# Kernel tuning notes

Measured on AMD Instinct MI355X. Metric: run time of the kernel, lower is better.

The kernel has to match this reference:

```python
import jax, jax.numpy as jnp
import numpy as np

IN_DIM, OUT_DIM = 256, 128
N_NODES, N_EDGES = 50000, 800000


def _glorot(key, shape):
    fan_in = shape[-1]
    return jax.random.normal(key, shape, dtype=jnp.float32) / jnp.sqrt(jnp.float32(fan_in))


def setup_inputs() -> dict:
    key = jax.random.key(0)
    ks = jax.random.split(key, 16)
    features1 = jax.random.normal(ks[0], (N_NODES, IN_DIM), dtype=jnp.float32)
    edge_index = jax.random.randint(ks[1], (2, N_EDGES), 0, N_NODES, dtype=jnp.int32)
    return {
        "features1": features1,
        "edge_index": edge_index,
        # encoder conv1: in->out
        "Wl_e1": _glorot(ks[2], (OUT_DIM, IN_DIM)), "bl_e1": jnp.zeros((OUT_DIM,), jnp.float32), "Wr_e1": _glorot(ks[3], (OUT_DIM, IN_DIM)),
        # encoder conv2: out->out
        "Wl_e2": _glorot(ks[4], (OUT_DIM, OUT_DIM)), "bl_e2": jnp.zeros((OUT_DIM,), jnp.float32), "Wr_e2": _glorot(ks[5], (OUT_DIM, OUT_DIM)),
        # fc: out->out
        "W_fc": _glorot(ks[6], (OUT_DIM, OUT_DIM)), "b_fc": jnp.zeros((OUT_DIM,), jnp.float32),
        # decoder conv1: out->out
        "Wl_d1": _glorot(ks[7], (OUT_DIM, OUT_DIM)), "bl_d1": jnp.zeros((OUT_DIM,), jnp.float32), "Wr_d1": _glorot(ks[8], (OUT_DIM, OUT_DIM)),
        # decoder conv2: out->in
        "Wl_d2": _glorot(ks[9], (IN_DIM, OUT_DIM)), "bl_d2": jnp.zeros((IN_DIM,), jnp.float32), "Wr_d2": _glorot(ks[10], (IN_DIM, OUT_DIM)),
    }


def _sage_conv(x, src, dst, inv_deg, Wl, bl, Wr):
    # mean aggregation of neighbor messages x[src] at destination nodes
    agg = jax.ops.segment_sum(x[src], dst, num_segments=N_NODES) * inv_deg  # [N, d_in]
    out = agg @ Wl.T + bl + x @ Wr.T  # lin_l(agg) + lin_r(x)
    # F.normalize(out, p=2, dim=-1)
    nrm = jnp.maximum(jnp.linalg.norm(out, axis=-1, keepdims=True), 1e-12)
    return out / nrm


def reference(features1, edge_index, Wl_e1, bl_e1, Wr_e1, Wl_e2, bl_e2, Wr_e2,
              W_fc, b_fc, Wl_d1, bl_d1, Wr_d1, Wl_d2, bl_d2, Wr_d2):
    src, dst = edge_index[0], edge_index[1]
    deg = jax.ops.segment_sum(jnp.ones((src.shape[0],), jnp.float32), dst, num_segments=N_NODES)
    inv_deg = (1.0 / jnp.maximum(deg, 1.0))[:, None]
    # encoder
    h = _sage_conv(features1, src, dst, inv_deg, Wl_e1, bl_e1, Wr_e1)
    x1 = _sage_conv(h, src, dst, inv_deg, Wl_e2, bl_e2, Wr_e2)
    # bottleneck linear
    x = x1 @ W_fc.T + b_fc
    # decoder
    h = _sage_conv(x, src, dst, inv_deg, Wl_d1, bl_d1, Wr_d1)
    x1_rec = _sage_conv(h, src, dst, inv_deg, Wl_d2, bl_d2, Wr_d2)
    return (x1, x1_rec)
```

## Files before the change

### kernel.cpp

```cpp
#include <hip/hip_runtime.h>
#include <hip/hip_bf16.h>
#include <math.h>

#define N_NODES 50000
#define N_EDGES 800000
#define SLOT_CAP 64

typedef short s16x8 __attribute__((ext_vector_type(8)));
typedef float f32x4 __attribute__((ext_vector_type(4)));

static __device__ __forceinline__ unsigned short f2bf(float x) {
    __hip_bfloat16 b = __float2bfloat16(x);
    return *(unsigned short*)&b;
}
static __device__ __forceinline__ float2 bfu2f2(unsigned int u) {
    __hip_bfloat162 b = *(__hip_bfloat162*)&u;
    return __bfloat1622float2(b);
}
static __device__ __forceinline__ unsigned int packbf2(float x, float y) {
    return (unsigned int)f2bf(x) | ((unsigned int)f2bf(y) << 16);
}

__global__ void k_fillslot(const int* __restrict__ src, const int* __restrict__ dst,
                           int* __restrict__ cnt, int* __restrict__ slots) {
    int e = blockIdx.x * blockDim.x + threadIdx.x;
    if (e >= N_EDGES) return;
    int d = dst[e];
    int pos = atomicAdd(&cnt[d], 1);
    if (pos < SLOT_CAP) slots[d * SLOT_CAP + pos] = src[e];
}

#define FEATN (N_NODES * 256)
#define O_WL_E1 (FEATN)
#define O_WR_E1 (FEATN + 32768)
#define O_WL_E2 (FEATN + 65536)
#define O_WR_E2 (FEATN + 81920)
#define O_W_FC  (FEATN + 98304)
#define O_WL_D1 (FEATN + 114688)
#define O_WR_D1 (FEATN + 131072)
#define O_D2    (FEATN + 147456)
#define PREP_TOT (FEATN + 212992)

__global__ __launch_bounds__(256) void k_prep(const float* __restrict__ feat,
                                              const float* __restrict__ wle1, const float* __restrict__ wre1,
                                              const float* __restrict__ wle2, const float* __restrict__ wre2,
                                              const float* __restrict__ wfc,
                                              const float* __restrict__ wld1, const float* __restrict__ wrd1,
                                              const float* __restrict__ wld2, const float* __restrict__ wrd2,
                                              unsigned short* __restrict__ dstp) {
    const int tot4 = PREP_TOT / 4;
    for (int i = blockIdx.x * blockDim.x + threadIdx.x; i < tot4; i += gridDim.x * blockDim.x) {
        int e = i * 4;
        const float* s;
        int off;
        if      (e < O_WL_E1) { s = feat; off = e; }
        else if (e < O_WR_E1) { s = wle1; off = e - O_WL_E1; }
        else if (e < O_WL_E2) { s = wre1; off = e - O_WR_E1; }
        else if (e < O_WR_E2) { s = wle2; off = e - O_WL_E2; }
        else if (e < O_W_FC)  { s = wre2; off = e - O_WR_E2; }
        else if (e < O_WL_D1) { s = wfc;  off = e - O_W_FC; }
        else if (e < O_WR_D1) { s = wld1; off = e - O_WL_D1; }
        else if (e < O_D2)    { s = wrd1; off = e - O_WR_D1; }
        else {
            int rel = e - O_D2;
            int row = rel >> 8, half = (rel >> 7) & 1, col = rel & 127;
            s = half ? wrd2 : wld2;
            off = row * 128 + col;
        }
        float4 v = *(const float4*)&s[off];
        ushort4 u;
        u.x = f2bf(v.x); u.y = f2bf(v.y); u.z = f2bf(v.z); u.w = f2bf(v.w);
        *(ushort4*)&dstp[e] = u;
    }
}

template <int K>
__global__ __launch_bounds__(256) void k_gmm2(const unsigned short* __restrict__ X,
                                              const unsigned short* __restrict__ W,
                                              const float* __restrict__ bias0,
                                              const float* __restrict__ bias1,
                                              unsigned short* __restrict__ Y,
                                              int N, int Ystride) {
    constexpr int CH = K / 8;
    __shared__ unsigned short Ws[128 * K];
    const unsigned short* Wsrc = W + (size_t)blockIdx.y * 128 * K;
    for (int idx = threadIdx.x; idx < 128 * CH; idx += 256) {
        int n = idx / CH, c = idx % CH;
        uint4 v = *(const uint4*)&Wsrc[n * K + c * 8];
        int cs = c ^ (n & 15);
        *(uint4*)&Ws[n * K + cs * 8] = v;
    }
    __syncthreads();

    const int wid = threadIdx.x >> 6, lane = threadIdx.x & 63;
    const int row0 = blockIdx.x * 128 + wid * 32;
    const int lrow = lane & 15;
    const int lk8  = lane >> 4;
    f32x4 acc[2][8] = {};

    for (int ks = 0; ks < K; ks += 32) {
        s16x8 a[2];
#pragma unroll
        for (int i = 0; i < 2; i++) {
            int r = row0 + i * 16 + lrow;
            s16x8 av = {};
            if (r < N) av = *(const s16x8*)&X[(size_t)r * K + ks + lk8 * 8];
            a[i] = av;
        }
#pragma unroll
        for (int nf = 0; nf < 8; nf++) {
            int n = nf * 16 + lrow;
            int c = (ks >> 3) + lk8;
            int cs = c ^ (n & 15);
            s16x8 b = *(const s16x8*)&Ws[n * K + cs * 8];
            acc[0][nf] = __builtin_amdgcn_mfma_f32_16x16x32_bf16(a[0], b, acc[0][nf], 0, 0, 0);
            acc[1][nf] = __builtin_amdgcn_mfma_f32_16x16x32_bf16(a[1], b, acc[1][nf], 0, 0, 0);
        }
    }

    const float* bias = (blockIdx.y == 0) ? bias0 : bias1;
    const int ccol = lane & 15, crow0 = (lane >> 4) * 4;
    const int ycol0 = blockIdx.y * 128;
#pragma unroll
    for (int nf = 0; nf < 8; nf++) {
        int lcol = nf * 16 + ccol;
        float bv = bias ? bias[lcol] : 0.0f;
#pragma unroll
        for (int i = 0; i < 2; i++) {
#pragma unroll
            for (int j = 0; j < 4; j++) {
                int grow = row0 + i * 16 + crow0 + j;
                if (grow < N) Y[(size_t)grow * Ystride + ycol0 + lcol] = f2bf(acc[i][nf][j] + bv);
            }
        }
    }
}

template <bool WRITE_F32>
__global__ __launch_bounds__(256) void k_aggfin4(const uint4* __restrict__ TP,
                                                 const int* __restrict__ slots,
                                                 const int* __restrict__ cnt,
                                                 float* __restrict__ OUTF,
                                                 uint4* __restrict__ OUTB,
                                                 int ostride4, int ooff4) {
    const int wave = (blockIdx.x * blockDim.x + threadIdx.x) >> 6;
    const int lane = threadIdx.x & 63;
    if (wave >= N_NODES) return;
    const int q = lane & 15, sub = lane >> 4;
    int deg = cnt[wave];
    deg = min(deg, SLOT_CAP);
    const int base = wave * SLOT_CAP;
    float acc[8] = {};
    int i = sub;
    for (; i + 4 < deg; i += 8) {
        int nb0 = slots[base + i], nb1 = slots[base + i + 4];
        uint4 v0 = TP[(size_t)nb0 * 32 + q];
        uint4 v1 = TP[(size_t)nb1 * 32 + q];
        float2 a0 = bfu2f2(v0.x), a1 = bfu2f2(v0.y), a2 = bfu2f2(v0.z), a3 = bfu2f2(v0.w);
        float2 b0 = bfu2f2(v1.x), b1 = bfu2f2(v1.y), b2 = bfu2f2(v1.z), b3 = bfu2f2(v1.w);
        acc[0] += a0.x + b0.x; acc[1] += a0.y + b0.y;
        acc[2] += a1.x + b1.x; acc[3] += a1.y + b1.y;
        acc[4] += a2.x + b2.x; acc[5] += a2.y + b2.y;
        acc[6] += a3.x + b3.x; acc[7] += a3.y + b3.y;
    }
    if (i < deg) {
        int nb = slots[base + i];
        uint4 v = TP[(size_t)nb * 32 + q];
        float2 a0 = bfu2f2(v.x), a1 = bfu2f2(v.y), a2 = bfu2f2(v.z), a3 = bfu2f2(v.w);
        acc[0] += a0.x; acc[1] += a0.y; acc[2] += a1.x; acc[3] += a1.y;
        acc[4] += a2.x; acc[5] += a2.y; acc[6] += a3.x; acc[7] += a3.y;
    }
#pragma unroll
    for (int k = 0; k < 8; k++) {
        acc[k] += __shfl_xor(acc[k], 16);
        acc[k] += __shfl_xor(acc[k], 32);
    }
    const float inv = 1.0f / fmaxf((float)deg, 1.0f);
    uint4 pv = TP[(size_t)wave * 32 + 16 + q];
    float2 p0 = bfu2f2(pv.x), p1 = bfu2f2(pv.y), p2 = bfu2f2(pv.z), p3 = bfu2f2(pv.w);
    float o[8];
    o[0] = p0.x + inv * acc[0]; o[1] = p0.y + inv * acc[1];
    o[2] = p1.x + inv * acc[2]; o[3] = p1.y + inv * acc[3];
    o[4] = p2.x + inv * acc[4]; o[5] = p2.y + inv * acc[5];
    o[6] = p3.x + inv * acc[6]; o[7] = p3.y + inv * acc[7];
    float ss = 0.0f;
#pragma unroll
    for (int k = 0; k < 8; k++) ss += o[k] * o[k];
    ss += __shfl_xor(ss, 1); ss += __shfl_xor(ss, 2);
    ss += __shfl_xor(ss, 4); ss += __shfl_xor(ss, 8);
    float r = 1.0f / fmaxf(sqrtf(ss), 1e-12f);
#pragma unroll
    for (int k = 0; k < 8; k++) o[k] *= r;
    if (lane < 16) {
        if constexpr (WRITE_F32) {
            ((float4*)OUTF)[(size_t)wave * 32 + q * 2]     = make_float4(o[0], o[1], o[2], o[3]);
            ((float4*)OUTF)[(size_t)wave * 32 + q * 2 + 1] = make_float4(o[4], o[5], o[6], o[7]);
        }
        uint4 u;
        u.x = packbf2(o[0], o[1]); u.y = packbf2(o[2], o[3]);
        u.z = packbf2(o[4], o[5]); u.w = packbf2(o[6], o[7]);
        OUTB[(size_t)wave * ostride4 + ooff4 + q] = u;
    }
}

__global__ __launch_bounds__(256) void k_agg4(const uint4* __restrict__ IN,
                                              const int* __restrict__ slots,
                                              const int* __restrict__ cnt,
                                              uint4* __restrict__ OUT,
                                              int istride4, int ioff4, int ostride4, int ooff4) {
    const int wave = (blockIdx.x * blockDim.x + threadIdx.x) >> 6;
    const int lane = threadIdx.x & 63;
    if (wave >= N_NODES) return;
    const int q = lane & 15, sub = lane >> 4;
    int deg = cnt[wave];
    deg = min(deg, SLOT_CAP);
    const int base = wave * SLOT_CAP;
    float acc[8] = {};
    int i = sub;
    for (; i + 4 < deg; i += 8) {
        int nb0 = slots[base + i], nb1 = slots[base + i + 4];
        uint4 v0 = IN[(size_t)nb0 * istride4 + ioff4 + q];
        uint4 v1 = IN[(size_t)nb1 * istride4 + ioff4 + q];
        float2 a0 = bfu2f2(v0.x), a1 = bfu2f2(v0.y), a2 = bfu2f2(v0.z), a3 = bfu2f2(v0.w);
        float2 b0 = bfu2f2(v1.x), b1 = bfu2f2(v1.y), b2 = bfu2f2(v1.z), b3 = bfu2f2(v1.w);
        acc[0] += a0.x + b0.x; acc[1] += a0.y + b0.y;
        acc[2] += a1.x + b1.x; acc[3] += a1.y + b1.y;
        acc[4] += a2.x + b2.x; acc[5] += a2.y + b2.y;
        acc[6] += a3.x + b3.x; acc[7] += a3.y + b3.y;
    }
    if (i < deg) {
        int nb = slots[base + i];
        uint4 v = IN[(size_t)nb * istride4 + ioff4 + q];
        float2 a0 = bfu2f2(v.x), a1 = bfu2f2(v.y), a2 = bfu2f2(v.z), a3 = bfu2f2(v.w);
        acc[0] += a0.x; acc[1] += a0.y; acc[2] += a1.x; acc[3] += a1.y;
        acc[4] += a2.x; acc[5] += a2.y; acc[6] += a3.x; acc[7] += a3.y;
    }
#pragma unroll
    for (int k = 0; k < 8; k++) {
        acc[k] += __shfl_xor(acc[k], 16);
        acc[k] += __shfl_xor(acc[k], 32);
    }
    const float inv = 1.0f / fmaxf((float)deg, 1.0f);
    if (lane < 16) {
        uint4 u;
        u.x = packbf2(inv * acc[0], inv * acc[1]);
        u.y = packbf2(inv * acc[2], inv * acc[3]);
        u.z = packbf2(inv * acc[4], inv * acc[5]);
        u.w = packbf2(inv * acc[6], inv * acc[7]);
        OUT[(size_t)wave * ostride4 + ooff4 + q] = u;
    }
}

__global__ __launch_bounds__(256) void k_norm256(const unsigned short* __restrict__ Rb,
                                                 float* __restrict__ OUT) {
    const int wave = (blockIdx.x * blockDim.x + threadIdx.x) >> 6;
    const int lane = threadIdx.x & 63;
    if (wave >= N_NODES) return;
    ushort4 v = ((const ushort4*)Rb)[(size_t)wave * 64 + lane];
    float x0 = __bfloat162float(*(__hip_bfloat16*)&v.x);
    float x1 = __bfloat162float(*(__hip_bfloat16*)&v.y);
    float x2 = __bfloat162float(*(__hip_bfloat16*)&v.z);
    float x3 = __bfloat162float(*(__hip_bfloat16*)&v.w);
    float ss = x0 * x0 + x1 * x1 + x2 * x2 + x3 * x3;
#pragma unroll
    for (int off = 32; off > 0; off >>= 1) ss += __shfl_xor(ss, off);
    float r = 1.0f / fmaxf(sqrtf(ss), 1e-12f);
    float4 o = make_float4(x0 * r, x1 * r, x2 * r, x3 * r);
    ((float4*)OUT)[(size_t)wave * 64 + lane] = o;
}

extern "C" void kernel_launch(void* const* d_in, const int* in_sizes, int n_in,
                              void* d_out, int out_size, void* d_ws, size_t ws_size,
                              hipStream_t stream) {
    const float* feat  = (const float*)d_in[0];
    const int*   ei    = (const int*)d_in[1];
    const int*   src   = ei;
    const int*   dst   = ei + N_EDGES;
    const float* Wl_e1 = (const float*)d_in[2];
    const float* bl_e1 = (const float*)d_in[3];
    const float* Wr_e1 = (const float*)d_in[4];
    const float* Wl_e2 = (const float*)d_in[5];
    const float* bl_e2 = (const float*)d_in[6];
    const float* Wr_e2 = (const float*)d_in[7];
    const float* W_fc  = (const float*)d_in[8];
    const float* b_fc  = (const float*)d_in[9];
    const float* Wl_d1 = (const float*)d_in[10];
    const float* bl_d1 = (const float*)d_in[11];
    const float* Wr_d1 = (const float*)d_in[12];
    const float* Wl_d2 = (const float*)d_in[13];
    const float* bl_d2 = (const float*)d_in[14];
    const float* Wr_d2 = (const float*)d_in[15];

    char* w = (char*)d_ws;
    auto alloc = [&](size_t bytes) -> void* {
        void* p = (void*)w;
        w += (bytes + 255) & ~(size_t)255;
        return p;
    };
    int* cnt   = (int*)alloc((size_t)N_NODES * 4);
    int* slots = (int*)alloc((size_t)N_NODES * SLOT_CAP * 4);
    unsigned short* bfpool = (unsigned short*)alloc((size_t)PREP_TOT * 2);
    unsigned short* TP   = (unsigned short*)alloc((size_t)N_NODES * 256 * 2);
    unsigned short* hb   = (unsigned short*)alloc((size_t)N_NODES * 128 * 2);
    unsigned short* x1b  = (unsigned short*)alloc((size_t)N_NODES * 128 * 2);
    unsigned short* X2   = (unsigned short*)alloc((size_t)N_NODES * 256 * 2);
    unsigned short* R1b  = (unsigned short*)alloc((size_t)N_NODES * 256 * 2);

    unsigned short* featb = bfpool;
    float* x1     = (float*)d_out;
    float* x1_rec = (float*)d_out + (size_t)N_NODES * 128;

    hipMemsetAsync(cnt, 0, (size_t)N_NODES * 4, stream);

    const int EB = (N_EDGES + 255) / 256;
    k_prep<<<2048, 256, 0, stream>>>(feat, Wl_e1, Wr_e1, Wl_e2, Wr_e2, W_fc, Wl_d1, Wr_d1, Wl_d2, Wr_d2, bfpool);
    k_fillslot<<<EB, 256, 0, stream>>>(src, dst, cnt, slots);

    const int NB128 = (N_NODES + 127) / 128;
    const int WPB   = (N_NODES * 64 + 255) / 256;

    k_gmm2<256><<<dim3(NB128, 2), 256, 0, stream>>>(featb, bfpool + O_WL_E1, nullptr, bl_e1, TP, N_NODES, 256);
    k_aggfin4<false><<<WPB, 256, 0, stream>>>((const uint4*)TP, slots, cnt, nullptr, (uint4*)hb, 16, 0);
    k_gmm2<128><<<dim3(NB128, 2), 256, 0, stream>>>(hb, bfpool + O_WL_E2, nullptr, bl_e2, TP, N_NODES, 256);
    k_aggfin4<true><<<WPB, 256, 0, stream>>>((const uint4*)TP, slots, cnt, x1, (uint4*)x1b, 16, 0);
    k_gmm2<128><<<dim3(NB128, 1), 256, 0, stream>>>(x1b, bfpool + O_W_FC, b_fc, nullptr, hb, N_NODES, 128);
    k_gmm2<128><<<dim3(NB128, 2), 256, 0, stream>>>(hb, bfpool + O_WL_D1, nullptr, bl_d1, TP, N_NODES, 256);
    k_aggfin4<false><<<WPB, 256, 0, stream>>>((const uint4*)TP, slots, cnt, nullptr, (uint4*)X2, 32, 16);
    k_agg4<<<WPB, 256, 0, stream>>>((const uint4*)X2, slots, cnt, (uint4*)X2, 32, 16, 32, 0);
    k_gmm2<256><<<dim3(NB128, 2), 256, 0, stream>>>(X2, bfpool + O_D2, bl_d2, bl_d2 + 128, R1b, N_NODES, 256);
    k_norm256<<<WPB, 256, 0, stream>>>(R1b, x1_rec);
}
```

Baseline: 341.3 us.

## Build compact CSR via bucketed counting sort and prefetch A tiles in GEMM

Replaces the fixed 64-slot per-node adjacency (filled with per-node global atomics) with a compact CSR. Edges are first bucketed into 256-node bins, then an exclusive scan produces bin offsets and a per-bin LDS counting sort writes row_start and csr. This cuts global atomic contention and makes neighbor index reads contiguous, at the cost of two extra kernel launches and extra passes over the edges. The GEMM kernel also double-buffers the A-operand register loads so the next k-slice is fetched while MFMAs run on the current one.

```diff
diff --git a/kernel.cpp b/kernel.cpp
--- a/kernel.cpp
+++ b/kernel.cpp
@@ -4,7 +4,8 @@
 
 #define N_NODES 50000
 #define N_EDGES 800000
-#define SLOT_CAP 64
+#define NBUCK ((N_NODES + 255) / 256)
+#define BCAP 6144
 
 typedef short s16x8 __attribute__((ext_vector_type(8)));
 typedef float f32x4 __attribute__((ext_vector_type(4)));
@@ -21,13 +22,70 @@
     return (unsigned int)f2bf(x) | ((unsigned int)f2bf(y) << 16);
 }
 
-__global__ void k_fillslot(const int* __restrict__ src, const int* __restrict__ dst,
-                           int* __restrict__ cnt, int* __restrict__ slots) {
+__global__ void k_bucket(const int* __restrict__ src, const int* __restrict__ dst,
+                         int* __restrict__ bcnt, unsigned int* __restrict__ bke) {
     int e = blockIdx.x * blockDim.x + threadIdx.x;
     if (e >= N_EDGES) return;
     int d = dst[e];
-    int pos = atomicAdd(&cnt[d], 1);
-    if (pos < SLOT_CAP) slots[d * SLOT_CAP + pos] = src[e];
+    int b = d >> 8;
+    int pos = atomicAdd(&bcnt[b], 1);
+    if (pos < BCAP) bke[b * BCAP + pos] = (unsigned int)src[e] | ((unsigned int)(d & 255) << 16);
+}
+
+__global__ __launch_bounds__(256) void k_bscan(const int* __restrict__ bcnt, int* __restrict__ bbase) {
+    __shared__ int lds[256];
+    int t = threadIdx.x;
+    int v = (t < NBUCK) ? min(bcnt[t], BCAP) : 0;
+    lds[t] = v;
+    __syncthreads();
+    for (int off = 1; off < 256; off <<= 1) {
+        int x = (t >= off) ? lds[t - off] : 0;
+        __syncthreads();
+        lds[t] += x;
+        __syncthreads();
+    }
+    if (t < NBUCK) bbase[t] = lds[t] - v;
+}
+
+__global__ __launch_bounds__(256) void k_binsort(const unsigned int* __restrict__ bke,
+                                                 const int* __restrict__ bcnt,
+                                                 const int* __restrict__ bbase,
+                                                 int* __restrict__ csr,
+                                                 int* __restrict__ row_start) {
+    __shared__ int cnt_l[256];
+    __shared__ int scan_l[256];
+    __shared__ int cursor[256];
+    __shared__ int stage[BCAP];
+    const int b = blockIdx.x;
+    const int t = threadIdx.x;
+    const int nb = min(bcnt[b], BCAP);
+    const unsigned int* ed = bke + (size_t)b * BCAP;
+    cnt_l[t] = 0;
+    __syncthreads();
+    for (int i = t; i < nb; i += 256) atomicAdd(&cnt_l[(ed[i] >> 16) & 255], 1);
+    __syncthreads();
+    int v = cnt_l[t];
+    scan_l[t] = v;
+    __syncthreads();
+    for (int off = 1; off < 256; off <<= 1) {
+        int x = (t >= off) ? scan_l[t - off] : 0;
+        __syncthreads();
+        scan_l[t] += x;
+        __syncthreads();
+    }
+    int excl = scan_l[t] - v;
+    cursor[t] = excl;
+    const int base = bbase[b];
+    int node = b * 256 + t;
+    if (node <= N_NODES) row_start[node] = base + excl;
+    __syncthreads();
+    for (int i = t; i < nb; i += 256) {
+        unsigned int u = ed[i];
+        int pos = atomicAdd(&cursor[(u >> 16) & 255], 1);
+        stage[pos] = (int)(u & 0xFFFF);
+    }
+    __syncthreads();
+    for (int i = t; i < nb; i += 256) csr[base + i] = stage[i];
 }
 
 #define FEATN (N_NODES * 256)
@@ -98,14 +156,24 @@
     const int lk8  = lane >> 4;
     f32x4 acc[2][8] = {};
 
+    s16x8 a_cur[2];
+#pragma unroll
+    for (int i = 0; i < 2; i++) {
+        int r = row0 + i * 16 + lrow;
+        s16x8 av = {};
+        if (r < N) av = *(const s16x8*)&X[(size_t)r * K + lk8 * 8];
+        a_cur[i] = av;
+    }
+
+#pragma unroll
     for (int ks = 0; ks < K; ks += 32) {
-        s16x8 a[2];
-#pragma unroll
-        for (int i = 0; i < 2; i++) {
-            int r = row0 + i * 16 + lrow;
-            s16x8 av = {};
-            if (r < N) av = *(const s16x8*)&X[(size_t)r * K + ks + lk8 * 8];
-            a[i] = av;
+        s16x8 a_nxt[2] = {};
+        if (ks + 32 < K) {
+#pragma unroll
+            for (int i = 0; i < 2; i++) {
+                int r = row0 + i * 16 + lrow;
+                if (r < N) a_nxt[i] = *(const s16x8*)&X[(size_t)r * K + ks + 32 + lk8 * 8];
+            }
         }
 #pragma unroll
         for (int nf = 0; nf < 8; nf++) {
@@ -113,9 +181,11 @@
             int c = (ks >> 3) + lk8;
             int cs = c ^ (n & 15);
             s16x8 b = *(const s16x8*)&Ws[n * K + cs * 8];
-            acc[0][nf] = __builtin_amdgcn_mfma_f32_16x16x32_bf16(a[0], b, acc[0][nf], 0, 0, 0);
-            acc[1][nf] = __builtin_amdgcn_mfma_f32_16x16x32_bf16(a[1], b, acc[1][nf], 0, 0, 0);
+            acc[0][nf] = __builtin_amdgcn_mfma_f32_16x16x32_bf16(a_cur[0], b, acc[0][nf], 0, 0, 0);
+            acc[1][nf] = __builtin_amdgcn_mfma_f32_16x16x32_bf16(a_cur[1], b, acc[1][nf], 0, 0, 0);
         }
+        a_cur[0] = a_nxt[0];
+        a_cur[1] = a_nxt[1];
     }
 
     const float* bias = (blockIdx.y == 0) ? bias0 : bias1;
@@ -138,8 +208,8 @@
 
 template <bool WRITE_F32>
 __global__ __launch_bounds__(256) void k_aggfin4(const uint4* __restrict__ TP,
-                                                 const int* __restrict__ slots,
-                                                 const int* __restrict__ cnt,
+                                                 const int* __restrict__ csr,
+                                                 const int* __restrict__ row_start,
                                                  float* __restrict__ OUTF,
                                                  uint4* __restrict__ OUTB,
                                                  int ostride4, int ooff4) {
@@ -147,13 +217,12 @@
     const int lane = threadIdx.x & 63;
     if (wave >= N_NODES) return;
     const int q = lane & 15, sub = lane >> 4;
-    int deg = cnt[wave];
-    deg = min(deg, SLOT_CAP);
-    const int base = wave * SLOT_CAP;
+    const int base = row_start[wave];
+    const int deg = row_start[wave + 1] - base;
     float acc[8] = {};
     int i = sub;
     for (; i + 4 < deg; i += 8) {
-        int nb0 = slots[base + i], nb1 = slots[base + i + 4];
+        int nb0 = csr[base + i], nb1 = csr[base + i + 4];
         uint4 v0 = TP[(size_t)nb0 * 32 + q];
         uint4 v1 = TP[(size_t)nb1 * 32 + q];
         float2 a0 = bfu2f2(v0.x), a1 = bfu2f2(v0.y), a2 = bfu2f2(v0.z), a3 = bfu2f2(v0.w);
@@ -164,7 +233,7 @@
         acc[6] += a3.x + b3.x; acc[7] += a3.y + b3.y;
     }
     if (i < deg) {
-        int nb = slots[base + i];
+        int nb = csr[base + i];
         uint4 v = TP[(size_t)nb * 32 + q];
         float2 a0 = bfu2f2(v.x), a1 = bfu2f2(v.y), a2 = bfu2f2(v.z), a3 = bfu2f2(v.w);
         acc[0] += a0.x; acc[1] += a0.y; acc[2] += a1.x; acc[3] += a1.y;
@@ -204,21 +273,20 @@
 }
 
 __global__ __launch_bounds__(256) void k_agg4(const uint4* __restrict__ IN,
-                                              const int* __restrict__ slots,
-                                              const int* __restrict__ cnt,
+                                              const int* __restrict__ csr,
+                                              const int* __restrict__ row_start,
                                               uint4* __restrict__ OUT,
                                               int istride4, int ioff4, int ostride4, int ooff4) {
     const int wave = (blockIdx.x * blockDim.x + threadIdx.x) >> 6;
     const int lane = threadIdx.x & 63;
     if (wave >= N_NODES) return;
     const int q = lane & 15, sub = lane >> 4;
-    int deg = cnt[wave];
-    deg = min(deg, SLOT_CAP);
-    const int base = wave * SLOT_CAP;
+    const int base = row_start[wave];
+    const int deg = row_start[wave + 1] - base;
     float acc[8] = {};
     int i = sub;
     for (; i + 4 < deg; i += 8) {
-        int nb0 = slots[base + i], nb1 = slots[base + i + 4];
+        int nb0 = csr[base + i], nb1 = csr[base + i + 4];
         uint4 v0 = IN[(size_t)nb0 * istride4 + ioff4 + q];
         uint4 v1 = IN[(size_t)nb1 * istride4 + ioff4 + q];
         float2 a0 = bfu2f2(v0.x), a1 = bfu2f2(v0.y), a2 = bfu2f2(v0.z), a3 = bfu2f2(v0.w);
@@ -229,7 +297,7 @@
         acc[6] += a3.x + b3.x; acc[7] += a3.y + b3.y;
     }
     if (i < deg) {
-        int nb = slots[base + i];
+        int nb = csr[base + i];
         uint4 v = IN[(size_t)nb * istride4 + ioff4 + q];
         float2 a0 = bfu2f2(v.x), a1 = bfu2f2(v.y), a2 = bfu2f2(v.z), a3 = bfu2f2(v.w);
         acc[0] += a0.x; acc[1] += a0.y; acc[2] += a1.x; acc[3] += a1.y;
@@ -297,8 +365,11 @@
         w += (bytes + 255) & ~(size_t)255;
         return p;
     };
-    int* cnt   = (int*)alloc((size_t)N_NODES * 4);
-    int* slots = (int*)alloc((size_t)N_NODES * SLOT_CAP * 4);
+    int* bcnt      = (int*)alloc((size_t)NBUCK * 4);
+    int* bbase     = (int*)alloc((size_t)NBUCK * 4);
+    unsigned int* bke = (unsigned int*)alloc((size_t)NBUCK * BCAP * 4);
+    int* csr       = (int*)alloc((size_t)N_EDGES * 4);
+    int* row_start = (int*)alloc((size_t)(N_NODES + 1) * 4);
     unsigned short* bfpool = (unsigned short*)alloc((size_t)PREP_TOT * 2);
     unsigned short* TP   = (unsigned short*)alloc((size_t)N_NODES * 256 * 2);
     unsigned short* hb   = (unsigned short*)alloc((size_t)N_NODES * 128 * 2);
@@ -310,23 +381,25 @@
     float* x1     = (float*)d_out;
     float* x1_rec = (float*)d_out + (size_t)N_NODES * 128;
 
-    hipMemsetAsync(cnt, 0, (size_t)N_NODES * 4, stream);
+    hipMemsetAsync(bcnt, 0, (size_t)NBUCK * 4, stream);
 
     const int EB = (N_EDGES + 255) / 256;
     k_prep<<<2048, 256, 0, stream>>>(feat, Wl_e1, Wr_e1, Wl_e2, Wr_e2, W_fc, Wl_d1, Wr_d1, Wl_d2, Wr_d2, bfpool);
-    k_fillslot<<<EB, 256, 0, stream>>>(src, dst, cnt, slots);
+    k_bucket<<<EB, 256, 0, stream>>>(src, dst, bcnt, bke);
+    k_bscan<<<1, 256, 0, stream>>>(bcnt, bbase);
+    k_binsort<<<NBUCK, 256, 0, stream>>>(bke, bcnt, bbase, csr, row_start);
 
     const int NB128 = (N_NODES + 127) / 128;
     const int WPB   = (N_NODES * 64 + 255) / 256;
 
     k_gmm2<256><<<dim3(NB128, 2), 256, 0, stream>>>(featb, bfpool + O_WL_E1, nullptr, bl_e1, TP, N_NODES, 256);
-    k_aggfin4<false><<<WPB, 256, 0, stream>>>((const uint4*)TP, slots, cnt, nullptr, (uint4*)hb, 16, 0);
+    k_aggfin4<false><<<WPB, 256, 0, stream>>>((const uint4*)TP, csr, row_start, nullptr, (uint4*)hb, 16, 0);
     k_gmm2<128><<<dim3(NB128, 2), 256, 0, stream>>>(hb, bfpool + O_WL_E2, nullptr, bl_e2, TP, N_NODES, 256);
-    k_aggfin4<true><<<WPB, 256, 0, stream>>>((const uint4*)TP, slots, cnt, x1, (uint4*)x1b, 16, 0);
+    k_aggfin4<true><<<WPB, 256, 0, stream>>>((const uint4*)TP, csr, row_start, x1, (uint4*)x1b, 16, 0);
     k_gmm2<128><<<dim3(NB128, 1), 256, 0, stream>>>(x1b, bfpool + O_W_FC, b_fc, nullptr, hb, N_NODES, 128);
     k_gmm2<128><<<dim3(NB128, 2), 256, 0, stream>>>(hb, bfpool + O_WL_D1, nullptr, bl_d1, TP, N_NODES, 256);
-    k_aggfin4<false><<<WPB, 256, 0, stream>>>((const uint4*)TP, slots, cnt, nullptr, (uint4*)X2, 32, 16);
-    k_agg4<<<WPB, 256, 0, stream>>>((const uint4*)X2, slots, cnt, (uint4*)X2, 32, 16, 32, 0);
+    k_aggfin4<false><<<WPB, 256, 0, stream>>>((const uint4*)TP, csr, row_start, nullptr, (uint4*)X2, 32, 16);
+    k_agg4<<<WPB, 256, 0, stream>>>((const uint4*)X2, csr, row_start, (uint4*)X2, 32, 16, 32, 0);
     k_gmm2<256><<<dim3(NB128, 2), 256, 0, stream>>>(X2, bfpool + O_D2, bl_d2, bl_d2 + 128, R1b, N_NODES, 256);
     k_norm256<<<WPB, 256, 0, stream>>>(R1b, x1_rec);
 }
```

Result: slower. 777.4 us (+127.8%).

## Fuse final decoder GEMM with L2 row normalization and prefetch A fragments

Applied to the files above, without the earlier changes.

Adds a GEMM kernel that computes all 256 output columns per block by loading the two weight halves into shared memory in turn. It then applies bias and row-wise L2 normalization in registers and writes fp32 output directly. This removes the bf16 intermediate round trip and the separate normalize kernel, and also avoids rounding the output to bf16 before normalizing. The existing GEMM also gets software prefetch of the next A k-slice. The new kernel holds twice as many accumulators and halves the number of blocks, so it risks register pressure and lower occupancy.

```diff
diff --git a/kernel.cpp b/kernel.cpp
--- a/kernel.cpp
+++ b/kernel.cpp
@@ -98,14 +98,24 @@
     const int lk8  = lane >> 4;
     f32x4 acc[2][8] = {};
 
+    s16x8 a_cur[2];
+#pragma unroll
+    for (int i = 0; i < 2; i++) {
+        int r = row0 + i * 16 + lrow;
+        s16x8 av = {};
+        if (r < N) av = *(const s16x8*)&X[(size_t)r * K + lk8 * 8];
+        a_cur[i] = av;
+    }
+
+#pragma unroll
     for (int ks = 0; ks < K; ks += 32) {
-        s16x8 a[2];
-#pragma unroll
-        for (int i = 0; i < 2; i++) {
-            int r = row0 + i * 16 + lrow;
-            s16x8 av = {};
-            if (r < N) av = *(const s16x8*)&X[(size_t)r * K + ks + lk8 * 8];
-            a[i] = av;
+        s16x8 a_nxt[2] = {};
+        if (ks + 32 < K) {
+#pragma unroll
+            for (int i = 0; i < 2; i++) {
+                int r = row0 + i * 16 + lrow;
+                if (r < N) a_nxt[i] = *(const s16x8*)&X[(size_t)r * K + ks + 32 + lk8 * 8];
+            }
         }
 #pragma unroll
         for (int nf = 0; nf < 8; nf++) {
@@ -113,9 +123,11 @@
             int c = (ks >> 3) + lk8;
             int cs = c ^ (n & 15);
             s16x8 b = *(const s16x8*)&Ws[n * K + cs * 8];
-            acc[0][nf] = __builtin_amdgcn_mfma_f32_16x16x32_bf16(a[0], b, acc[0][nf], 0, 0, 0);
-            acc[1][nf] = __builtin_amdgcn_mfma_f32_16x16x32_bf16(a[1], b, acc[1][nf], 0, 0, 0);
-        }
+            acc[0][nf] = __builtin_amdgcn_mfma_f32_16x16x32_bf16(a_cur[0], b, acc[0][nf], 0, 0, 0);
+            acc[1][nf] = __builtin_amdgcn_mfma_f32_16x16x32_bf16(a_cur[1], b, acc[1][nf], 0, 0, 0);
+        }
+        a_cur[0] = a_nxt[0];
+        a_cur[1] = a_nxt[1];
     }
 
     const float* bias = (blockIdx.y == 0) ? bias0 : bias1;
@@ -134,6 +146,102 @@
             }
         }
     }
+}
+
+__global__ __launch_bounds__(256) void k_gmmn(const unsigned short* __restrict__ X,
+                                              const unsigned short* __restrict__ W,
+                                              const float* __restrict__ bias,
+                                              float* __restrict__ OUT, int N) {
+    __shared__ unsigned short Ws[128 * 256];
+    const int wid = threadIdx.x >> 6, lane = threadIdx.x & 63;
+    const int row0 = blockIdx.x * 128 + wid * 32;
+    const int lrow = lane & 15;
+    const int lk8  = lane >> 4;
+    const int ccol = lane & 15, crow0 = (lane >> 4) * 4;
+    f32x4 acc[2][2][8] = {};
+
+#pragma unroll
+    for (int half = 0; half < 2; half++) {
+        __syncthreads();
+        const unsigned short* Wsrc = W + (size_t)half * 128 * 256;
+        for (int idx = threadIdx.x; idx < 128 * 32; idx += 256) {
+            int n = idx / 32, c = idx % 32;
+            uint4 v = *(const uint4*)&Wsrc[n * 256 + c * 8];
+            int cs = c ^ (n & 15);
+            *(uint4*)&Ws[n * 256 + cs * 8] = v;
+        }
+        __syncthreads();
+
+        s16x8 a_cur[2];
+#pragma unroll
+        for (int i = 0; i < 2; i++) {
+            int r = row0 + i * 16 + lrow;
+            s16x8 av = {};
+            if (r < N) av = *(const s16x8*)&X[(size_t)r * 256 + lk8 * 8];
+            a_cur[i] = av;
+        }
+#pragma unroll
+        for (int ks = 0; ks < 256; ks += 32) {
+            s16x8 a_nxt[2] = {};
+            if (ks + 32 < 256) {
+#pragma unroll
+                for (int i = 0; i < 2; i++) {
+                    int r = row0 + i * 16 + lrow;
+                    if (r < N) a_nxt[i] = *(const s16x8*)&X[(size_t)r * 256 + ks + 32 + lk8 * 8];
+                }
+            }
+#pragma unroll
+            for (int nf = 0; nf < 8; nf++) {
+                int n = nf * 16 + lrow;
+                int c = (ks >> 3) + lk8;
+                int cs = c ^ (n & 15);
+                s16x8 b = *(const s16x8*)&Ws[n * 256 + cs * 8];
+                acc[half][0][nf] = __builtin_amdgcn_mfma_f32_16x16x32_bf16(a_cur[0], b, acc[half][0][nf], 0, 0, 0);
+                acc[half][1][nf] = __builtin_amdgcn_mfma_f32_16x16x32_bf16(a_cur[1], b, acc[half][1][nf], 0, 0, 0);
+            }
+            a_cur[0] = a_nxt[0];
+            a_cur[1] = a_nxt[1];
+        }
+    }
+
+#pragma unroll
+    for (int half = 0; half < 2; half++)
+#pragma unroll
+        for (int nf = 0; nf < 8; nf++) {
+            float bv = bias[half * 128 + nf * 16 + ccol];
+#pragma unroll
+            for (int i = 0; i < 2; i++)
+#pragma unroll
+                for (int j = 0; j < 4; j++) acc[half][i][nf][j] += bv;
+        }
+    float rs[2][4];
+#pragma unroll
+    for (int i = 0; i < 2; i++)
+#pragma unroll
+        for (int j = 0; j < 4; j++) {
+            float ss = 0.0f;
+#pragma unroll
+            for (int half = 0; half < 2; half++)
+#pragma unroll
+                for (int nf = 0; nf < 8; nf++) ss += acc[half][i][nf][j] * acc[half][i][nf][j];
+            ss += __shfl_xor(ss, 1); ss += __shfl_xor(ss, 2);
+            ss += __shfl_xor(ss, 4); ss += __shfl_xor(ss, 8);
+            rs[i][j] = 1.0f / fmaxf(sqrtf(ss), 1e-12f);
+        }
+#pragma unroll
+    for (int i = 0; i < 2; i++)
+#pragma unroll
+        for (int j = 0; j < 4; j++) {
+            int grow = row0 + i * 16 + crow0 + j;
+            if (grow < N) {
+                float r = rs[i][j];
+#pragma unroll
+                for (int half = 0; half < 2; half++)
+#pragma unroll
+                    for (int nf = 0; nf < 8; nf++)
+                        OUT[(size_t)grow * 256 + half * 128 + nf * 16 + ccol] = acc[half][i][nf][j] * r;
+            }
+        }
 }
 
 template <bool WRITE_F32>
@@ -251,24 +359,6 @@
     }
 }
 
-__global__ __launch_bounds__(256) void k_norm256(const unsigned short* __restrict__ Rb,
-                                                 float* __restrict__ OUT) {
-    const int wave = (blockIdx.x * blockDim.x + threadIdx.x) >> 6;
-    const int lane = threadIdx.x & 63;
-    if (wave >= N_NODES) return;
-    ushort4 v = ((const ushort4*)Rb)[(size_t)wave * 64 + lane];
-    float x0 = __bfloat162float(*(__hip_bfloat16*)&v.x);
-    float x1 = __bfloat162float(*(__hip_bfloat16*)&v.y);
-    float x2 = __bfloat162float(*(__hip_bfloat16*)&v.z);
-    float x3 = __bfloat162float(*(__hip_bfloat16*)&v.w);
-    float ss = x0 * x0 + x1 * x1 + x2 * x2 + x3 * x3;
-#pragma unroll
-    for (int off = 32; off > 0; off >>= 1) ss += __shfl_xor(ss, off);
-    float r = 1.0f / fmaxf(sqrtf(ss), 1e-12f);
-    float4 o = make_float4(x0 * r, x1 * r, x2 * r, x3 * r);
-    ((float4*)OUT)[(size_t)wave * 64 + lane] = o;
-}
-
 extern "C" void kernel_launch(void* const* d_in, const int* in_sizes, int n_in,
                               void* d_out, int out_size, void* d_ws, size_t ws_size,
                               hipStream_t stream) {
@@ -304,7 +394,6 @@
     unsigned short* hb   = (unsigned short*)alloc((size_t)N_NODES * 128 * 2);
     unsigned short* x1b  = (unsigned short*)alloc((size_t)N_NODES * 128 * 2);
     unsigned short* X2   = (unsigned short*)alloc((size_t)N_NODES * 256 * 2);
-    unsigned short* R1b  = (unsigned short*)alloc((size_t)N_NODES * 256 * 2);
 
     unsigned short* featb = bfpool;
     float* x1     = (float*)d_out;
@@ -327,6 +416,5 @@
     k_gmm2<128><<<dim3(NB128, 2), 256, 0, stream>>>(hb, bfpool + O_WL_D1, nullptr, bl_d1, TP, N_NODES, 256);
     k_aggfin4<false><<<WPB, 256, 0, stream>>>((const uint4*)TP, slots, cnt, nullptr, (uint4*)X2, 32, 16);
     k_agg4<<<WPB, 256, 0, stream>>>((const uint4*)X2, slots, cnt, (uint4*)X2, 32, 16, 32, 0);
-    k_gmm2<256><<<dim3(NB128, 2), 256, 0, stream>>>(X2, bfpool + O_D2, bl_d2, bl_d2 + 128, R1b, N_NODES, 256);
-    k_norm256<<<WPB, 256, 0, stream>>>(R1b, x1_rec);
-}
+    k_gmmn<<<NB128, 256, 0, stream>>>(X2, bfpool + O_D2, bl_d2, x1_rec, N_NODES);
+}
```

After: 345.2 us. No clear change (+1.2%).
